# Performance work log

Hardware: AMD Instinct MI355X
Metric: run time of the kernel (lower is better)

Reference implementation:

```python
import jax, jax.numpy as jnp
import numpy as np

N_NODES = 50000


def _graph_conv(x, edges, W0, b0, W1, b1):
    # Symmetric (undirected) message passing: each edge (a,b) sends x[b]->a and x[a]->b.
    src = jnp.concatenate([edges[:, 0], edges[:, 1]])  # [2E]
    dst = jnp.concatenate([edges[:, 1], edges[:, 0]])  # [2E]
    deg = jax.ops.segment_sum(jnp.ones_like(dst, dtype=x.dtype), dst, num_segments=N_NODES)
    deg = jnp.maximum(deg, 1.0)  # avoid div-by-zero for isolated nodes
    agg = jax.ops.segment_sum(x[src], dst, num_segments=N_NODES) / deg[:, None]  # [N, F]
    # self transform + normalized-neighbor transform
    return x @ W0 + b0 + agg @ W1 + b1


def setup_inputs() -> dict:
    key = jax.random.key(0)
    ks = jax.random.split(key, 10)
    feats = [256, 512, 256]  # [in] + hidden + [out]
    inp = {
        "vert_features": jax.random.normal(ks[0], (N_NODES, feats[0]), dtype=jnp.float32),
        "edges": jax.random.randint(ks[1], (400000, 2), 0, N_NODES, dtype=jnp.int64),
    }
    kidx = 2
    for l, (fi, fo) in enumerate(zip(feats[:-1], feats[1:])):
        s = 1.0 / np.sqrt(fi)
        inp[f"W0_{l}"] = jax.random.normal(ks[kidx], (fi, fo), dtype=jnp.float32) * s
        inp[f"b0_{l}"] = jnp.zeros((fo,), dtype=jnp.float32)
        inp[f"W1_{l}"] = jax.random.normal(ks[kidx + 1], (fi, fo), dtype=jnp.float32) * s
        inp[f"b1_{l}"] = jnp.zeros((fo,), dtype=jnp.float32)
        kidx += 2
    return inp


def reference(vert_features, edges, W0_0, b0_0, W1_0, b1_0, W0_1, b0_1, W1_1, b1_1):
    # layer 0 + ReLU
    x = _graph_conv(vert_features, edges, W0_0, b0_0, W1_0, b1_0)
    x = jax.nn.relu(x)
    # final layer (no activation)
    x = _graph_conv(x, edges, W0_1, b0_1, W1_1, b1_1)
    return x
```

## Files before the change

### kernel.cpp

```cpp
#include <hip/hip_runtime.h>
#include <stdint.h>

typedef __bf16  bf16x8 __attribute__((ext_vector_type(8)));
typedef float   f32x4  __attribute__((ext_vector_type(4)));
typedef float   f32x2  __attribute__((ext_vector_type(2)));
typedef unsigned short u16x8 __attribute__((ext_vector_type(8)));

__device__ __forceinline__ unsigned short f2bf(float f) {
  unsigned int u = __float_as_uint(f);
  u += 0x7fffu + ((u >> 16) & 1u);
  return (unsigned short)(u >> 16);
}
__device__ __forceinline__ float bflo(unsigned int v) { return __uint_as_float(v << 16); }
__device__ __forceinline__ float bfhi(unsigned int v) { return __uint_as_float(v & 0xffff0000u); }

__device__ __forceinline__ f32x2 fp8_dec_lo(unsigned int u) { return __builtin_amdgcn_cvt_pk_f32_fp8(u, false); }
__device__ __forceinline__ f32x2 fp8_dec_hi(unsigned int u) { return __builtin_amdgcn_cvt_pk_f32_fp8(u, true); }
__device__ __forceinline__ unsigned int fp8_enc_lo(float a, float b, unsigned int old) {
  return __builtin_amdgcn_cvt_pk_fp8_f32(a, b, old, false);
}
__device__ __forceinline__ unsigned int fp8_enc_hi(float a, float b, unsigned int old) {
  return __builtin_amdgcn_cvt_pk_fp8_f32(a, b, old, true);
}

__device__ __forceinline__ void glds16(const unsigned short* g, unsigned short* l) {
  __builtin_amdgcn_global_load_lds(
      (const __attribute__((address_space(1))) unsigned int*)g,
      (__attribute__((address_space(3))) unsigned int*)l, 16, 0, 0);
}

__device__ __forceinline__ int edges_are_i64(const int* __restrict__ eg) {
  return (eg[1] | eg[3] | eg[5] | eg[7]) == 0;
}

__global__ void phase1_kernel(const float* __restrict__ x, unsigned short* __restrict__ A0,
                              unsigned char* __restrict__ Xq, int n,
                              const int* __restrict__ eg, int* __restrict__ deg, int E,
                              const float* __restrict__ W00, const float* __restrict__ W10,
                              const float* __restrict__ W01, const float* __restrict__ W11,
                              const float* __restrict__ b00, const float* __restrict__ b10,
                              const float* __restrict__ b01, const float* __restrict__ b11,
                              unsigned short* __restrict__ Bt1, unsigned short* __restrict__ Bt2,
                              float* __restrict__ bias1, float* __restrict__ bias2) {
  const int i = blockIdx.x * 256 + threadIdx.x;
  if (i < n * 64) {
    const int row = i >> 6, c4 = i & 63;
    const float4 v = ((const float4*)x)[i];
    ushort4 o;
    o.x = f2bf(v.x); o.y = f2bf(v.y); o.z = f2bf(v.z); o.w = f2bf(v.w);
    *(ushort4*)&A0[(size_t)row * 512 + c4 * 4] = o;
    unsigned int q = 0;
    q = fp8_enc_lo(v.x, v.y, q);
    q = fp8_enc_hi(v.z, v.w, q);
    *(unsigned int*)&Xq[(size_t)row * 256 + c4 * 4] = q;
  }
  if (i < 512 * 512) {
    const int nn = i >> 9, k = i & 511;
    const float v1 = (k < 256) ? W00[k * 512 + nn] : W10[(k - 256) * 512 + nn];
    Bt1[i] = f2bf(v1);
    const float v2 = (nn < 256) ? W01[k * 256 + nn] : W11[k * 256 + (nn - 256)];
    Bt2[i] = f2bf(v2);
    if (i < 512) {
      bias1[i] = b00[i] + b10[i];
      bias2[i] = (i < 256) ? (b01[i] + b11[i]) : 0.f;
    }
  }
  if (i < E) {
    int a, b;
    if (edges_are_i64(eg)) { a = eg[4 * i]; b = eg[4 * i + 2]; }
    else                   { a = eg[2 * i]; b = eg[2 * i + 1]; }
    if ((unsigned)a < (unsigned)n && (unsigned)b < (unsigned)n) {
      atomicAdd(&deg[a], 1);
      atomicAdd(&deg[b], 1);
    }
  }
}

__global__ void block_sum_kernel(const int* __restrict__ deg, int* __restrict__ bsum, int n) {
  const int t = threadIdx.x;
  const int i = blockIdx.x * 1024 + t;
  int v = (i < n) ? deg[i] : 0;
  #pragma unroll
  for (int d = 32; d > 0; d >>= 1) v += __shfl_xor(v, d);
  __shared__ int ws[16];
  if ((t & 63) == 0) ws[t >> 6] = v;
  __syncthreads();
  if (t < 16) {
    int s = ws[t];
    #pragma unroll
    for (int d = 1; d < 16; d <<= 1) s += __shfl_xor(s, d);
    if (t == 0) bsum[blockIdx.x] = s;
  }
}

__global__ void scan_bsum_kernel(int* __restrict__ bsum, int* __restrict__ off, int nb, int n) {
  const int l = threadIdx.x;
  int v = (l < nb) ? bsum[l] : 0;
  const int orig = v;
  #pragma unroll
  for (int d = 1; d < 64; d <<= 1) {
    int u = __shfl_up(v, d);
    if (l >= d) v += u;
  }
  if (l < nb) bsum[l] = v - orig;
  if (l == nb - 1) off[n] = v;
}

__global__ void scan_final_kernel(const int* __restrict__ deg, const int* __restrict__ bsum,
                                  int* __restrict__ off, float* __restrict__ invd,
                                  int* __restrict__ curp, int n) {
  const int t = threadIdx.x;
  const int i = blockIdx.x * 1024 + t;
  const int lane = t & 63, wid = t >> 6;
  const int v = (i < n) ? deg[i] : 0;
  int s = v;
  #pragma unroll
  for (int d = 1; d < 64; d <<= 1) {
    int u = __shfl_up(s, d);
    if (lane >= d) s += u;
  }
  __shared__ int ws[16];
  if (lane == 63) ws[wid] = s;
  __syncthreads();
  if (t < 16) {
    int w = ws[t];
    #pragma unroll
    for (int d = 1; d < 16; d <<= 1) {
      int u = __shfl_up(w, d);
      if (t >= d) w += u;
    }
    ws[t] = w;
  }
  __syncthreads();
  const int add = (wid > 0) ? ws[wid - 1] : 0;
  const int incl = s + add;
  if (i < n) {
    off[i] = bsum[blockIdx.x] + incl - v;
    invd[i] = 1.f / (float)(v > 1 ? v : 1);
    curp[i] = 0;
  }
}

__global__ void fill_kernel(const int* __restrict__ eg,
                            const int* __restrict__ off, int* __restrict__ cur,
                            int* __restrict__ adj, int E, int n) {
  const int e = blockIdx.x * 256 + threadIdx.x;
  if (e >= E) return;
  int a, b;
  if (edges_are_i64(eg)) { a = eg[4 * e]; b = eg[4 * e + 2]; }
  else                   { a = eg[2 * e]; b = eg[2 * e + 1]; }
  if ((unsigned)a >= (unsigned)n || (unsigned)b >= (unsigned)n) return;
  int p = atomicAdd(&cur[b], 1); adj[off[b] + p] = a;
  int q = atomicAdd(&cur[a], 1); adj[off[a] + q] = b;
}

template<int MODE>
__global__ __launch_bounds__(256) void agg_fp8_kernel(
    const unsigned char* __restrict__ Tq, unsigned short* A0w, float* out,
    const int* __restrict__ adj, const int* __restrict__ off,
    const float* __restrict__ invd, int n) {
  const int node = blockIdx.x * 4 + (threadIdx.x >> 6);
  if (node >= n) return;
  const int lane = threadIdx.x & 63;
  const int rq = lane >> 4;
  const int cq = lane & 15;
  const int s = off[node], e = off[node + 1];
  float acc[16];
  #pragma unroll
  for (int i = 0; i < 16; ++i) acc[i] = 0.f;

  for (int base = s; base < e; base += 64) {
    const int cnt = min(64, e - base);
    const int idxv = (lane < cnt) ? adj[base + lane] : 0;
    for (int j = 0; j < cnt; j += 8) {
      const int s0 = j + rq, s1 = j + 4 + rq;
      const int r0 = __shfl(idxv, s0), r1 = __shfl(idxv, s1);
      uint4 v0 = make_uint4(0u, 0u, 0u, 0u), v1 = v0;
      if (s0 < cnt) v0 = *(const uint4*)&Tq[(size_t)r0 * 256 + cq * 16];
      if (s1 < cnt) v1 = *(const uint4*)&Tq[(size_t)r1 * 256 + cq * 16];
      #pragma unroll
      for (int h = 0; h < 2; ++h) {
        const uint4 v = h ? v1 : v0;
        f32x2 a, b;
        a = fp8_dec_lo(v.x); b = fp8_dec_hi(v.x);
        acc[0] += a[0];  acc[1] += a[1];  acc[2] += b[0];  acc[3] += b[1];
        a = fp8_dec_lo(v.y); b = fp8_dec_hi(v.y);
        acc[4] += a[0];  acc[5] += a[1];  acc[6] += b[0];  acc[7] += b[1];
        a = fp8_dec_lo(v.z); b = fp8_dec_hi(v.z);
        acc[8] += a[0];  acc[9] += a[1];  acc[10] += b[0]; acc[11] += b[1];
        a = fp8_dec_lo(v.w); b = fp8_dec_hi(v.w);
        acc[12] += a[0]; acc[13] += a[1]; acc[14] += b[0]; acc[15] += b[1];
      }
    }
  }
  #pragma unroll
  for (int i = 0; i < 16; ++i) {
    acc[i] += __shfl_xor(acc[i], 16);
    acc[i] += __shfl_xor(acc[i], 32);
  }
  if (rq == 0) {
    const float sc = invd[node];
    if (MODE == 0) {
      u16x8 o0, o1;
      #pragma unroll
      for (int k = 0; k < 8; ++k) { o0[k] = f2bf(acc[k] * sc); o1[k] = f2bf(acc[8 + k] * sc); }
      *(u16x8*)&A0w[(size_t)node * 512 + 256 + cq * 16] = o0;
      *(u16x8*)&A0w[(size_t)node * 512 + 256 + cq * 16 + 8] = o1;
    } else {
      float* po = &out[(size_t)node * 256 + cq * 16];
      #pragma unroll
      for (int k = 0; k < 4; ++k) {
        float4 pv = ((float4*)po)[k];
        pv.x += sc * acc[4 * k + 0]; pv.y += sc * acc[4 * k + 1];
        pv.z += sc * acc[4 * k + 2]; pv.w += sc * acc[4 * k + 3];
        ((float4*)po)[k] = pv;
      }
    }
  }
}

__global__ __launch_bounds__(512, 1) void fused_gemm_kernel(
    const unsigned short* __restrict__ A, const unsigned short* __restrict__ B1,
    const unsigned short* __restrict__ B2,
    const float* __restrict__ bias1, const float* __restrict__ bias2,
    float* __restrict__ Pout, unsigned char* __restrict__ Zq, int M_real) {
  __shared__ __attribute__((aligned(16))) char smem[163840];
  unsigned short* sA  = (unsigned short*)smem;
  unsigned short* sB  = (unsigned short*)(smem + 32768);
  unsigned short* Hl  = (unsigned short*)smem;
  unsigned short* sB2 = (unsigned short*)(smem + 131072);
  const int t = threadIdx.x;
  const int lane = t & 63;
  const int wid = t >> 6;
  const int wr = wid >> 2;
  const int wc = wid & 3;
  const int m0 = blockIdx.x * 128;

  f32x4 acc1[2][4][4];
  #pragma unroll
  for (int c = 0; c < 2; ++c)
    #pragma unroll
    for (int m = 0; m < 4; ++m)
      #pragma unroll
      for (int n = 0; n < 4; ++n)
        acc1[c][m][n] = f32x4{0.f, 0.f, 0.f, 0.f};

  #pragma unroll
  for (int nc1 = 0; nc1 < 2; ++nc1) {
    auto stageA = [&](int buf, int kt) {
      #pragma unroll
      for (int i = 0; i < 2; ++i) {
        const int row = (t >> 3) + i * 64;
        const int c = (t & 7) ^ (row & 7);
        glds16(A + (size_t)(m0 + row) * 512 + kt * 64 + c * 8,
               &sA[buf * 8192 + (i * 512 + t) * 8]);
      }
      #pragma unroll
      for (int i = 0; i < 4; ++i) {
        const int row = (t >> 3) + i * 64;
        const int c = (t & 7) ^ (row & 7);
        glds16(B1 + (size_t)(nc1 * 256 + row) * 512 + kt * 64 + c * 8,
               &sB[buf * 16384 + (i * 512 + t) * 8]);
      }
    };
    stageA(0, 0);
    __syncthreads();
    #pragma unroll 1
    for (int kt = 0; kt < 8; ++kt) {
      if (kt < 7) stageA((kt + 1) & 1, kt + 1);
      const int buf = kt & 1;
      #pragma unroll
      for (int kk = 0; kk < 2; ++kk) {
        bf16x8 aF[4], bF[4];
        #pragma unroll
        for (int m = 0; m < 4; ++m) {
          const int row = wr * 64 + m * 16 + (lane & 15);
          const int sl = (kk * 4 + (lane >> 4)) ^ (row & 7);
          aF[m] = *(const bf16x8*)&sA[buf * 8192 + row * 64 + sl * 8];
        }
        #pragma unroll
        for (int n = 0; n < 4; ++n) {
          const int rl = wc * 64 + n * 16 + (lane & 15);
          const int sl = (kk * 4 + (lane >> 4)) ^ (rl & 7);
          bF[n] = *(const bf16x8*)&sB[buf * 16384 + rl * 64 + sl * 8];
        }
        #pragma unroll
        for (int m = 0; m < 4; ++m)
          #pragma unroll
          for (int n = 0; n < 4; ++n)
            acc1[nc1][m][n] = __builtin_amdgcn_mfma_f32_16x16x32_bf16(aF[m], bF[n], acc1[nc1][m][n], 0, 0, 0);
      }
      __syncthreads();
    }
  }

  #pragma unroll
  for (int nc1 = 0; nc1 < 2; ++nc1) {
    #pragma unroll
    for (int n = 0; n < 4; ++n) {
      const int col = nc1 * 256 + wc * 64 + n * 16 + (lane & 15);
      const float bc = bias1[col];
      #pragma unroll
      for (int m = 0; m < 4; ++m) {
        #pragma unroll
        for (int r = 0; r < 4; ++r) {
          const int row = wr * 64 + m * 16 + (lane >> 4) * 4 + r;
          float y = acc1[nc1][m][n][r] + bc;
          y = y > 0.f ? y : 0.f;
          Hl[row * 512 + (((col >> 3) ^ (row & 7)) << 3) + (col & 7)] = f2bf(y);
        }
      }
    }
  }
  __syncthreads();

  f32x4 acc2[4][4][2];
  #pragma unroll
  for (int g = 0; g < 4; ++g)
    #pragma unroll
    for (int m = 0; m < 4; ++m)
      #pragma unroll
      for (int n = 0; n < 2; ++n)
        acc2[g][m][n] = f32x4{0.f, 0.f, 0.f, 0.f};

  #pragma unroll 1
  for (int kt = 0; kt < 16; ++kt) {
    __syncthreads();
    #pragma unroll
    for (int i = 0; i < 4; ++i) {
      const int idx = i * 512 + t;
      const int row = idx >> 2;
      const int c = (idx & 3) ^ ((row >> 1) & 3);
      glds16(B2 + (size_t)row * 512 + kt * 32 + c * 8, &sB2[idx * 8]);
    }
    __syncthreads();
    bf16x8 aF2[4];
    #pragma unroll
    for (int m = 0; m < 4; ++m) {
      const int hr = wr * 64 + m * 16 + (lane & 15);
      const int chk = (kt * 4 + (lane >> 4)) ^ (hr & 7);
      aF2[m] = *(const bf16x8*)&Hl[hr * 512 + chk * 8];
    }
    #pragma unroll
    for (int g = 0; g < 4; ++g) {
      bf16x8 bF2[2];
      #pragma unroll
      for (int n = 0; n < 2; ++n) {
        const int rl = g * 128 + wc * 32 + n * 16 + (lane & 15);
        const int sl = (lane >> 4) ^ ((rl >> 1) & 3);
        bF2[n] = *(const bf16x8*)&sB2[rl * 32 + sl * 8];
      }
      #pragma unroll
      for (int m = 0; m < 4; ++m)
        #pragma unroll
        for (int n = 0; n < 2; ++n)
          acc2[g][m][n] = __builtin_amdgcn_mfma_f32_16x16x32_bf16(aF2[m], bF2[n], acc2[g][m][n], 0, 0, 0);
    }
  }
  __syncthreads();

  #pragma unroll
  for (int g = 0; g < 2; ++g) {
    #pragma unroll
    for (int n = 0; n < 2; ++n) {
      const int gcol = g * 128 + wc * 32 + n * 16 + (lane & 15);
      const float bc = bias2[gcol];
      #pragma unroll
      for (int m = 0; m < 4; ++m) {
        #pragma unroll
        for (int r = 0; r < 4; ++r) {
          const int grow = m0 + wr * 64 + m * 16 + (lane >> 4) * 4 + r;
          if (grow < M_real) Pout[(size_t)grow * 256 + gcol] = acc2[g][m][n][r] + bc;
        }
      }
    }
  }

  #pragma unroll
  for (int g = 2; g < 4; ++g) {
    unsigned short* rep = sB2;
    #pragma unroll
    for (int n = 0; n < 2; ++n) {
      const int lcol = wc * 32 + n * 16 + (lane & 15);
      #pragma unroll
      for (int m = 0; m < 4; ++m) {
        #pragma unroll
        for (int r = 0; r < 4; ++r) {
          const int lr = wr * 64 + m * 16 + (lane >> 4) * 4 + r;
          rep[lr * 128 + (lcol ^ (((lr >> 2) & 7) << 4))] = f2bf(acc2[g][m][n][r]);
        }
      }
    }
    __syncthreads();
    #pragma unroll
    for (int p = 0; p < 4; ++p) {
      const int idx = p * 512 + t;
      const int tr = idx >> 4;
      const int cb = (idx & 15) * 8;
      const uint4 v = *(const uint4*)&rep[tr * 128 + (cb ^ (((tr >> 2) & 7) << 4))];
      unsigned int lo = 0, hi = 0;
      lo = fp8_enc_lo(bflo(v.x), bfhi(v.x), lo);
      lo = fp8_enc_hi(bflo(v.y), bfhi(v.y), lo);
      hi = fp8_enc_lo(bflo(v.z), bfhi(v.z), hi);
      hi = fp8_enc_hi(bflo(v.w), bfhi(v.w), hi);
      *(uint2*)&Zq[(size_t)(m0 + tr) * 256 + (g - 2) * 128 + cb] = make_uint2(lo, hi);
    }
    __syncthreads();
  }
}

extern "C" void kernel_launch(void* const* d_in, const int* in_sizes, int n_in,
                              void* d_out, int out_size, void* d_ws, size_t ws_size,
                              hipStream_t stream) {
  const float* x   = (const float*)d_in[0];
  const int* edges = (const int*)d_in[1];
  const float* W00 = (const float*)d_in[2];
  const float* b00 = (const float*)d_in[3];
  const float* W10 = (const float*)d_in[4];
  const float* b10 = (const float*)d_in[5];
  const float* W01 = (const float*)d_in[6];
  const float* b01 = (const float*)d_in[7];
  const float* W11 = (const float*)d_in[8];
  const float* b11 = (const float*)d_in[9];
  float* out = (float*)d_out;

  const int n = in_sizes[0] / 256;
  const int E = in_sizes[1] / 2;
  const int nstrip = (n + 127) / 128;
  const int Mp = nstrip * 128;

  char* p = (char*)d_ws;
  auto alloc = [&](size_t bytes) { char* r = p; p += (bytes + 255) & ~(size_t)255; return r; };
  unsigned short* A0  = (unsigned short*)alloc((size_t)Mp * 512 * 2);
  unsigned char*  Xq  = (unsigned char*)alloc((size_t)Mp * 256);
  unsigned char*  Zq  = (unsigned char*)alloc((size_t)Mp * 256);
  unsigned short* Bt1 = (unsigned short*)alloc(512 * 512 * 2);
  unsigned short* Bt2 = (unsigned short*)alloc(512 * 512 * 2);
  float* bias1 = (float*)alloc(512 * 4);
  float* bias2 = (float*)alloc(512 * 4);
  int*   deg   = (int*)alloc((size_t)n * 4);
  int*   curp  = (int*)alloc((size_t)n * 4);
  int*   off   = (int*)alloc((size_t)(n + 1) * 4);
  int*   bsum  = (int*)alloc(256 * 4);
  float* invd  = (float*)alloc((size_t)n * 4);
  int*   adj   = (int*)alloc((size_t)2 * E * 4);

  hipMemsetAsync(deg, 0, (size_t)n * 4, stream);

  const int p1_blocks = (n * 64 + 255) / 256;
  phase1_kernel<<<p1_blocks, 256, 0, stream>>>(x, A0, Xq, n, edges, deg, E,
                                               W00, W10, W01, W11, b00, b10, b01, b11,
                                               Bt1, Bt2, bias1, bias2);

  const int nb = (n + 1023) / 1024;
  block_sum_kernel<<<nb, 1024, 0, stream>>>(deg, bsum, n);
  scan_bsum_kernel<<<1, 64, 0, stream>>>(bsum, off, nb, n);
  scan_final_kernel<<<nb, 1024, 0, stream>>>(deg, bsum, off, invd, curp, n);
  fill_kernel<<<(E + 255) / 256, 256, 0, stream>>>(edges, off, curp, adj, E, n);

  agg_fp8_kernel<0><<<(n + 3) / 4, 256, 0, stream>>>(Xq, A0, nullptr, adj, off, invd, n);

  fused_gemm_kernel<<<nstrip, 512, 0, stream>>>(A0, Bt1, Bt2, bias1, bias2, out, Zq, n);

  agg_fp8_kernel<1><<<(n + 3) / 4, 256, 0, stream>>>(Zq, nullptr, out, adj, off, invd, n);
}
```

Measured before the change: 277.4 us.

## Replace LDS-staged fused GEMM with direct-global fragment loads on 64-row strips

The fused two-layer GEMM now loads A and weight fragments directly from global memory into registers instead of staging them through double-buffered LDS with async global-to-LDS copies. Row strips shrink to 64 and blocks to 256 threads with two blocks per CU, keeping only the hidden activations in LDS. The aim is to drop LDS staging overhead and barriers and raise occupancy. The cost is losing LDS reuse, so each wave re-reads weights and A from L2/global with strided 16-byte accesses.

```diff
diff --git a/kernel.cpp b/kernel.cpp
--- a/kernel.cpp
+++ b/kernel.cpp
@@ -21,12 +21,6 @@
 }
 __device__ __forceinline__ unsigned int fp8_enc_hi(float a, float b, unsigned int old) {
   return __builtin_amdgcn_cvt_pk_fp8_f32(a, b, old, true);
-}
-
-__device__ __forceinline__ void glds16(const unsigned short* g, unsigned short* l) {
-  __builtin_amdgcn_global_load_lds(
-      (const __attribute__((address_space(1))) unsigned int*)g,
-      (__attribute__((address_space(3))) unsigned int*)l, 16, 0, 0);
 }
 
 __device__ __forceinline__ int edges_are_i64(const int* __restrict__ eg) {
@@ -219,193 +213,131 @@
   }
 }
 
-__global__ __launch_bounds__(512, 1) void fused_gemm_kernel(
+__global__ __launch_bounds__(256, 2) void fused_gemm_kernel(
     const unsigned short* __restrict__ A, const unsigned short* __restrict__ B1,
     const unsigned short* __restrict__ B2,
     const float* __restrict__ bias1, const float* __restrict__ bias2,
     float* __restrict__ Pout, unsigned char* __restrict__ Zq, int M_real) {
-  __shared__ __attribute__((aligned(16))) char smem[163840];
-  unsigned short* sA  = (unsigned short*)smem;
-  unsigned short* sB  = (unsigned short*)(smem + 32768);
-  unsigned short* Hl  = (unsigned short*)smem;
-  unsigned short* sB2 = (unsigned short*)(smem + 131072);
+  __shared__ unsigned short Hl[64 * 512];
   const int t = threadIdx.x;
   const int lane = t & 63;
-  const int wid = t >> 6;
-  const int wr = wid >> 2;
-  const int wc = wid & 3;
-  const int m0 = blockIdx.x * 128;
-
-  f32x4 acc1[2][4][4];
-  #pragma unroll
-  for (int c = 0; c < 2; ++c)
+  const int w = t >> 6;
+  const int l15 = lane & 15;
+  const int lk = lane >> 4;
+  const int m0 = blockIdx.x * 64;
+
+  f32x4 acc1[4][8];
+  #pragma unroll
+  for (int m = 0; m < 4; ++m)
+    #pragma unroll
+    for (int nn = 0; nn < 8; ++nn)
+      acc1[m][nn] = f32x4{0.f, 0.f, 0.f, 0.f};
+
+  #pragma unroll 1
+  for (int kt = 0; kt < 16; ++kt) {
+    bf16x8 aF[4], bF[8];
     #pragma unroll
     for (int m = 0; m < 4; ++m)
-      #pragma unroll
-      for (int n = 0; n < 4; ++n)
-        acc1[c][m][n] = f32x4{0.f, 0.f, 0.f, 0.f};
-
-  #pragma unroll
-  for (int nc1 = 0; nc1 < 2; ++nc1) {
-    auto stageA = [&](int buf, int kt) {
-      #pragma unroll
-      for (int i = 0; i < 2; ++i) {
-        const int row = (t >> 3) + i * 64;
-        const int c = (t & 7) ^ (row & 7);
-        glds16(A + (size_t)(m0 + row) * 512 + kt * 64 + c * 8,
-               &sA[buf * 8192 + (i * 512 + t) * 8]);
-      }
-      #pragma unroll
-      for (int i = 0; i < 4; ++i) {
-        const int row = (t >> 3) + i * 64;
-        const int c = (t & 7) ^ (row & 7);
-        glds16(B1 + (size_t)(nc1 * 256 + row) * 512 + kt * 64 + c * 8,
-               &sB[buf * 16384 + (i * 512 + t) * 8]);
-      }
-    };
-    stageA(0, 0);
-    __syncthreads();
-    #pragma unroll 1
-    for (int kt = 0; kt < 8; ++kt) {
-      if (kt < 7) stageA((kt + 1) & 1, kt + 1);
-      const int buf = kt & 1;
-      #pragma unroll
-      for (int kk = 0; kk < 2; ++kk) {
-        bf16x8 aF[4], bF[4];
-        #pragma unroll
-        for (int m = 0; m < 4; ++m) {
-          const int row = wr * 64 + m * 16 + (lane & 15);
-          const int sl = (kk * 4 + (lane >> 4)) ^ (row & 7);
-          aF[m] = *(const bf16x8*)&sA[buf * 8192 + row * 64 + sl * 8];
-        }
-        #pragma unroll
-        for (int n = 0; n < 4; ++n) {
-          const int rl = wc * 64 + n * 16 + (lane & 15);
-          const int sl = (kk * 4 + (lane >> 4)) ^ (rl & 7);
-          bF[n] = *(const bf16x8*)&sB[buf * 16384 + rl * 64 + sl * 8];
-        }
-        #pragma unroll
-        for (int m = 0; m < 4; ++m)
-          #pragma unroll
-          for (int n = 0; n < 4; ++n)
-            acc1[nc1][m][n] = __builtin_amdgcn_mfma_f32_16x16x32_bf16(aF[m], bF[n], acc1[nc1][m][n], 0, 0, 0);
-      }
-      __syncthreads();
-    }
-  }
-
-  #pragma unroll
-  for (int nc1 = 0; nc1 < 2; ++nc1) {
-    #pragma unroll
-    for (int n = 0; n < 4; ++n) {
-      const int col = nc1 * 256 + wc * 64 + n * 16 + (lane & 15);
-      const float bc = bias1[col];
+      aF[m] = *(const bf16x8*)&A[(size_t)(m0 + m * 16 + l15) * 512 + kt * 32 + lk * 8];
+    #pragma unroll
+    for (int nn = 0; nn < 8; ++nn)
+      bF[nn] = *(const bf16x8*)&B1[(size_t)(w * 128 + nn * 16 + l15) * 512 + kt * 32 + lk * 8];
+    #pragma unroll
+    for (int m = 0; m < 4; ++m)
+      #pragma unroll
+      for (int nn = 0; nn < 8; ++nn)
+        acc1[m][nn] = __builtin_amdgcn_mfma_f32_16x16x32_bf16(aF[m], bF[nn], acc1[m][nn], 0, 0, 0);
+  }
+
+  #pragma unroll
+  for (int nn = 0; nn < 8; ++nn) {
+    const int col = w * 128 + nn * 16 + l15;
+    const float bc = bias1[col];
+    #pragma unroll
+    for (int m = 0; m < 4; ++m) {
+      #pragma unroll
+      for (int r = 0; r < 4; ++r) {
+        const int row = m * 16 + lk * 4 + r;
+        float y = acc1[m][nn][r] + bc;
+        y = y > 0.f ? y : 0.f;
+        Hl[row * 512 + (((col >> 3) ^ (row & 7)) << 3) + (col & 7)] = f2bf(y);
+      }
+    }
+  }
+  __syncthreads();
+
+  f32x4 acc2[4][8];
+  #pragma unroll
+  for (int m = 0; m < 4; ++m)
+    #pragma unroll
+    for (int nn = 0; nn < 8; ++nn)
+      acc2[m][nn] = f32x4{0.f, 0.f, 0.f, 0.f};
+
+  #pragma unroll 1
+  for (int kt = 0; kt < 16; ++kt) {
+    bf16x8 aF2[4], bF2[8];
+    #pragma unroll
+    for (int m = 0; m < 4; ++m) {
+      const int row = m * 16 + l15;
+      const int chk = (kt * 4 + lk) ^ (row & 7);
+      aF2[m] = *(const bf16x8*)&Hl[row * 512 + chk * 8];
+    }
+    #pragma unroll
+    for (int nn = 0; nn < 8; ++nn)
+      bF2[nn] = *(const bf16x8*)&B2[(size_t)(w * 128 + nn * 16 + l15) * 512 + kt * 32 + lk * 8];
+    #pragma unroll
+    for (int m = 0; m < 4; ++m)
+      #pragma unroll
+      for (int nn = 0; nn < 8; ++nn)
+        acc2[m][nn] = __builtin_amdgcn_mfma_f32_16x16x32_bf16(aF2[m], bF2[nn], acc2[m][nn], 0, 0, 0);
+  }
+  __syncthreads();
+
+  if (w < 2) {
+    #pragma unroll
+    for (int nn = 0; nn < 8; ++nn) {
+      const int gcol = w * 128 + nn * 16 + l15;
+      const float bc = bias2[gcol];
       #pragma unroll
       for (int m = 0; m < 4; ++m) {
         #pragma unroll
         for (int r = 0; r < 4; ++r) {
-          const int row = wr * 64 + m * 16 + (lane >> 4) * 4 + r;
-          float y = acc1[nc1][m][n][r] + bc;
-          y = y > 0.f ? y : 0.f;
-          Hl[row * 512 + (((col >> 3) ^ (row & 7)) << 3) + (col & 7)] = f2bf(y);
+          const int grow = m0 + m * 16 + lk * 4 + r;
+          if (grow < M_real) Pout[(size_t)grow * 256 + gcol] = acc2[m][nn][r] + bc;
         }
       }
     }
-  }
-  __syncthreads();
-
-  f32x4 acc2[4][4][2];
-  #pragma unroll
-  for (int g = 0; g < 4; ++g)
-    #pragma unroll
-    for (int m = 0; m < 4; ++m)
-      #pragma unroll
-      for (int n = 0; n < 2; ++n)
-        acc2[g][m][n] = f32x4{0.f, 0.f, 0.f, 0.f};
-
-  #pragma unroll 1
-  for (int kt = 0; kt < 16; ++kt) {
-    __syncthreads();
-    #pragma unroll
-    for (int i = 0; i < 4; ++i) {
-      const int idx = i * 512 + t;
-      const int row = idx >> 2;
-      const int c = (idx & 3) ^ ((row >> 1) & 3);
-      glds16(B2 + (size_t)row * 512 + kt * 32 + c * 8, &sB2[idx * 8]);
-    }
-    __syncthreads();
-    bf16x8 aF2[4];
-    #pragma unroll
-    for (int m = 0; m < 4; ++m) {
-      const int hr = wr * 64 + m * 16 + (lane & 15);
-      const int chk = (kt * 4 + (lane >> 4)) ^ (hr & 7);
-      aF2[m] = *(const bf16x8*)&Hl[hr * 512 + chk * 8];
-    }
-    #pragma unroll
-    for (int g = 0; g < 4; ++g) {
-      bf16x8 bF2[2];
-      #pragma unroll
-      for (int n = 0; n < 2; ++n) {
-        const int rl = g * 128 + wc * 32 + n * 16 + (lane & 15);
-        const int sl = (lane >> 4) ^ ((rl >> 1) & 3);
-        bF2[n] = *(const bf16x8*)&sB2[rl * 32 + sl * 8];
-      }
-      #pragma unroll
-      for (int m = 0; m < 4; ++m)
-        #pragma unroll
-        for (int n = 0; n < 2; ++n)
-          acc2[g][m][n] = __builtin_amdgcn_mfma_f32_16x16x32_bf16(aF2[m], bF2[n], acc2[g][m][n], 0, 0, 0);
-    }
-  }
-  __syncthreads();
-
-  #pragma unroll
-  for (int g = 0; g < 2; ++g) {
-    #pragma unroll
-    for (int n = 0; n < 2; ++n) {
-      const int gcol = g * 128 + wc * 32 + n * 16 + (lane & 15);
-      const float bc = bias2[gcol];
+  } else {
+    unsigned short* rep = &Hl[(w - 2) * 8192];
+    #pragma unroll
+    for (int nn = 0; nn < 8; ++nn) {
+      const int lcol = nn * 16 + l15;
       #pragma unroll
       for (int m = 0; m < 4; ++m) {
         #pragma unroll
         for (int r = 0; r < 4; ++r) {
-          const int grow = m0 + wr * 64 + m * 16 + (lane >> 4) * 4 + r;
-          if (grow < M_real) Pout[(size_t)grow * 256 + gcol] = acc2[g][m][n][r] + bc;
+          const int lr = m * 16 + lk * 4 + r;
+          rep[lr * 128 + (lcol ^ (((lr >> 2) & 7) << 4))] = f2bf(acc2[m][nn][r]);
         }
       }
     }
   }
-
-  #pragma unroll
-  for (int g = 2; g < 4; ++g) {
-    unsigned short* rep = sB2;
-    #pragma unroll
-    for (int n = 0; n < 2; ++n) {
-      const int lcol = wc * 32 + n * 16 + (lane & 15);
-      #pragma unroll
-      for (int m = 0; m < 4; ++m) {
-        #pragma unroll
-        for (int r = 0; r < 4; ++r) {
-          const int lr = wr * 64 + m * 16 + (lane >> 4) * 4 + r;
-          rep[lr * 128 + (lcol ^ (((lr >> 2) & 7) << 4))] = f2bf(acc2[g][m][n][r]);
-        }
-      }
-    }
-    __syncthreads();
-    #pragma unroll
-    for (int p = 0; p < 4; ++p) {
-      const int idx = p * 512 + t;
-      const int tr = idx >> 4;
-      const int cb = (idx & 15) * 8;
-      const uint4 v = *(const uint4*)&rep[tr * 128 + (cb ^ (((tr >> 2) & 7) << 4))];
-      unsigned int lo = 0, hi = 0;
-      lo = fp8_enc_lo(bflo(v.x), bfhi(v.x), lo);
-      lo = fp8_enc_hi(bflo(v.y), bfhi(v.y), lo);
-      hi = fp8_enc_lo(bflo(v.z), bfhi(v.z), hi);
-      hi = fp8_enc_hi(bflo(v.w), bfhi(v.w), hi);
-      *(uint2*)&Zq[(size_t)(m0 + tr) * 256 + (g - 2) * 128 + cb] = make_uint2(lo, hi);
-    }
-    __syncthreads();
+  __syncthreads();
+
+  #pragma unroll
+  for (int p = 0; p < 8; ++p) {
+    const int idx = p * 256 + t;
+    const int tr = idx >> 5;
+    const int it = idx & 31;
+    const int g = it >> 4;
+    const int cb = (it & 15) * 8;
+    const uint4 v = *(const uint4*)&Hl[g * 8192 + tr * 128 + (cb ^ (((tr >> 2) & 7) << 4))];
+    unsigned int lo = 0, hi = 0;
+    lo = fp8_enc_lo(bflo(v.x), bfhi(v.x), lo);
+    lo = fp8_enc_hi(bflo(v.y), bfhi(v.y), lo);
+    hi = fp8_enc_lo(bflo(v.z), bfhi(v.z), hi);
+    hi = fp8_enc_hi(bflo(v.w), bfhi(v.w), hi);
+    *(uint2*)&Zq[(size_t)(m0 + tr) * 256 + g * 128 + cb] = make_uint2(lo, hi);
   }
 }
 
@@ -426,8 +358,8 @@
 
   const int n = in_sizes[0] / 256;
   const int E = in_sizes[1] / 2;
-  const int nstrip = (n + 127) / 128;
-  const int Mp = nstrip * 128;
+  const int nstrip = (n + 63) / 64;
+  const int Mp = nstrip * 64;
 
   char* p = (char*)d_ws;
   auto alloc = [&](size_t bytes) { char* r = p; p += (bytes + 255) & ~(size_t)255; return r; };
@@ -460,7 +392,7 @@
 
   agg_fp8_kernel<0><<<(n + 3) / 4, 256, 0, stream>>>(Xq, A0, nullptr, adj, off, invd, n);
 
-  fused_gemm_kernel<<<nstrip, 512, 0, stream>>>(A0, Bt1, Bt2, bias1, bias2, out, Zq, n);
+  fused_gemm_kernel<<<nstrip, 256, 0, stream>>>(A0, Bt1, Bt2, bias1, bias2, out, Zq, n);
 
   agg_fp8_kernel<1><<<(n + 3) / 4, 256, 0, stream>>>(Zq, nullptr, out, adj, off, invd, n);
 }
```

New measurement: 353.0 us. 1.27x slower.
